# Kernel optimization log

Measured on AMD Instinct MI355X. Metric: run time of the kernel, lower is better.

## Reference

```python
import jax, jax.numpy as jnp
import numpy as np

DIM = 1024
HEADS = 16
HEAD_DIM = DIM // HEADS
SCALE = DIM ** -0.5  # note: original uses full dim, not head_dim


def setup_inputs() -> dict:
    key = jax.random.key(0)
    k1, k2, k3, k4 = jax.random.split(key, 4)
    x = jax.random.normal(k1, (4, 2048, DIM), dtype=jnp.float32)
    # nn.Linear(dim, 3*dim, bias=False): weight [3*dim, dim]; y = x @ W.T
    w_qkv = jax.random.normal(k2, (3 * DIM, DIM), dtype=jnp.float32) * (DIM ** -0.5)
    w_out = jax.random.normal(k3, (DIM, DIM), dtype=jnp.float32) * (DIM ** -0.5)
    b_out = jax.random.normal(k4, (DIM,), dtype=jnp.float32) * 0.01
    return {"x": x, "w_qkv": w_qkv, "w_out": w_out, "b_out": b_out}


def reference(x, w_qkv, w_out, b_out):
    b, n, d = x.shape
    qkv = jnp.einsum('bnd,ed->bne', x, w_qkv)  # [b, n, 3*dim]
    # rearrange 'b n (qkv h d) -> qkv b h n d'
    qkv = qkv.reshape(b, n, 3, HEADS, HEAD_DIM).transpose(2, 0, 3, 1, 4)
    q, k, v = qkv[0], qkv[1], qkv[2]
    dots = jnp.einsum('bhid,bhjd->bhij', q, k) * SCALE
    attn = jax.nn.softmax(dots, axis=-1)
    out = jnp.einsum('bhij,bhjd->bhid', attn, v)
    out = out.transpose(0, 2, 1, 3).reshape(b, n, d)  # b h n d -> b n (h d)
    return jnp.einsum('bnd,ed->bne', out, w_out) + b_out
```

## Files before the change

### kernel.cpp

```cpp
#include <hip/hip_runtime.h>
#include <stdint.h>
#include <stddef.h>

typedef _Float16 f16;
typedef __attribute__((ext_vector_type(8))) _Float16 f16x8;
typedef __attribute__((ext_vector_type(4))) _Float16 f16x4;
typedef __attribute__((ext_vector_type(2))) _Float16 f16x2;
typedef __attribute__((ext_vector_type(4))) float f32x4;

#define DINL __device__ __forceinline__

DINL f16x2 pkrtz(float a, float b) {
    return __builtin_bit_cast(f16x2, __builtin_amdgcn_cvt_pkrtz(a, b));
}

DINL void async_cp16(void* lds, const void* gmem) {
    __builtin_amdgcn_global_load_lds(
        (const __attribute__((address_space(1))) void*)(uintptr_t)gmem,
        (__attribute__((address_space(3))) void*)(uint32_t)(uintptr_t)lds,
        16, 0, 0);
}

__global__ void cast_fused(const float* __restrict__ x, f16* __restrict__ xh,
                           const float* __restrict__ wq, f16* __restrict__ wqh,
                           const float* __restrict__ wo, f16* __restrict__ woh,
                           float qs) {
    int stride = gridDim.x * blockDim.x;
    for (int i = blockIdx.x * blockDim.x + threadIdx.x; i < 3145728; i += stride) {
        const float4* src; f16x4* dst; float s = 1.f;
        if (i < 2097152)      { src = (const float4*)x  + i;            dst = (f16x4*)xh  + i; }
        else if (i < 2883584) { int j = i - 2097152; src = (const float4*)wq + j; dst = (f16x4*)wqh + j;
                                if (j < 262144) s = qs; }
        else                  { int j = i - 2883584; src = (const float4*)wo + j; dst = (f16x4*)woh + j; }
        float4 v = *src;
        f16x4 h = { (f16)(v.x * s), (f16)(v.y * s), (f16)(v.z * s), (f16)(v.w * s) };
        *dst = h;
    }
}

template <typename TC, bool HAS_BIAS>
__global__ __launch_bounds__(512, 2) void gemm8p(
    const f16* __restrict__ A, const f16* __restrict__ B,
    TC* __restrict__ C, const float* __restrict__ bias,
    int M, int N, int K)
{
    __shared__ __align__(16) char lds[98304];

    const int tid  = threadIdx.x;
    const int lane = tid & 63;
    const int wave = tid >> 6;
    const int rlo  = lane & 15;
    const int hi   = lane >> 4;
    const int wm   = wave & 3;
    const int wn   = wave >> 2;
    const int bm   = blockIdx.y * 256;
    const int bn   = blockIdx.x * 128;

    const int rA = tid >> 2;
    const int lc = (tid & 3) ^ ((tid >> 3) & 3);
    const f16* pA0 = A + (size_t)(bm + rA) * K + lc * 8;
    const f16* pA1 = A + (size_t)(bm + 128 + rA) * K + lc * 8;
    const f16* pB  = B + (size_t)(bn + rA) * K + lc * 8;
    const uint32_t dst0 = (uint32_t)tid * 16;
    const uint32_t dst1 = 8192u + (uint32_t)tid * 16;
    const uint32_t dstB = (uint32_t)tid * 16;

    const int fsw = (rlo >> 1) & 3;
    uint32_t afb[4], bfb[4];
#pragma unroll
    for (int m = 0; m < 4; ++m)
        afb[m] = (uint32_t)(wm * 64 + m * 16 + rlo) * 64 + (uint32_t)((hi ^ fsw) << 4);
#pragma unroll
    for (int n = 0; n < 4; ++n)
        bfb[n] = (uint32_t)(wn * 64 + n * 16 + rlo) * 64 + (uint32_t)((hi ^ fsw) << 4);

    f32x4 acc[4][4] = {};
    const int NP = K >> 5;

    auto stage = [&](int sg) {
        const uint32_t sa = (uint32_t)(sg & 3) << 14;
        const uint32_t sb = 65536u + ((uint32_t)(sg & 3) << 13);
        async_cp16(lds + sa + dst0, pA0);
        async_cp16(lds + sa + dst1, pA1);
        async_cp16(lds + sb + dstB, pB);
        pA0 += 32; pA1 += 32; pB += 32;
    };

    stage(0); stage(1); stage(2);

    for (int g = 0; g < NP; ++g) {
        if (g + 2 < NP)      asm volatile("s_waitcnt vmcnt(6)" ::: "memory");
        else if (g + 1 < NP) asm volatile("s_waitcnt vmcnt(3)" ::: "memory");
        else                 asm volatile("s_waitcnt vmcnt(0)" ::: "memory");
        __builtin_amdgcn_s_barrier();
        asm volatile("" ::: "memory");
        __builtin_amdgcn_sched_barrier(0);

        if (g + 3 < NP) stage(g + 3);

        const uint32_t sa = (uint32_t)(g & 3) << 14;
        const uint32_t sb = 65536u + ((uint32_t)(g & 3) << 13);

        f16x8 af[4], bf[4];
#pragma unroll
        for (int m = 0; m < 4; ++m)
            af[m] = *(const f16x8*)(lds + sa + afb[m]);
#pragma unroll
        for (int n = 0; n < 4; ++n)
            bf[n] = *(const f16x8*)(lds + sb + bfb[n]);

        __builtin_amdgcn_s_setprio(1);
#pragma unroll
        for (int m = 0; m < 4; ++m)
#pragma unroll
            for (int n = 0; n < 4; ++n)
                acc[m][n] = __builtin_amdgcn_mfma_f32_16x16x32_f16(af[m], bf[n], acc[m][n], 0, 0, 0);
        __builtin_amdgcn_s_setprio(0);
    }

#pragma unroll
    for (int n = 0; n < 4; ++n) {
        const int gc = bn + wn * 64 + n * 16 + rlo;
        float bv = 0.f;
        if constexpr (HAS_BIAS) bv = bias[gc];
#pragma unroll
        for (int m = 0; m < 4; ++m) {
            const int gr0 = bm + wm * 64 + m * 16 + (hi << 2);
#pragma unroll
            for (int r = 0; r < 4; ++r) {
                float v = acc[m][n][r] + bv;
                if constexpr (sizeof(TC) == 4) C[(size_t)(gr0 + r) * N + gc] = v;
                else                           C[(size_t)(gr0 + r) * N + gc] = (f16)v;
            }
        }
    }
}

__global__ __launch_bounds__(256) void transpose_v(const f16* __restrict__ qkv, f16* __restrict__ vt) {
    __shared__ float T[64][65];
    const int bid = blockIdx.x, bh = bid >> 5, st = bid & 31;
    const int b = bh >> 4, h = bh & 15, s0 = st * 64;
    const int tid = threadIdx.x;
    const int rs = tid >> 2, c0 = (tid & 3) * 16;
    const f16* src = &qkv[(size_t)(b * 2048 + s0 + rs) * 3072 + 2048 + h * 64 + c0];
    f16x8 v0 = ((const f16x8*)src)[0], v1 = ((const f16x8*)src)[1];
#pragma unroll
    for (int e = 0; e < 8; ++e) { T[rs][c0 + e] = (float)v0[e]; T[rs][c0 + 8 + e] = (float)v1[e]; }
    __syncthreads();
    const int rd = tid >> 2, k0 = (tid & 3) * 16;
    f16x8 w0, w1;
#pragma unroll
    for (int e = 0; e < 8; ++e) { w0[e] = (f16)T[k0 + e][rd]; w1[e] = (f16)T[k0 + 8 + e][rd]; }
    f16* dst = &vt[(size_t)(bh * 64 + rd) * 2048 + s0 + k0];
    ((f16x8*)dst)[0] = w0; ((f16x8*)dst)[1] = w1;
}

DINL int phi_row(int r) {
    return (r & 32) | ((r & 12) << 1) | ((r & 16) >> 2) | (r & 3);
}

__global__ __launch_bounds__(256, 4) void attn_mfma(
    const f16* __restrict__ qkv, const f16* __restrict__ vt, f16* __restrict__ out)
{
    constexpr int TD = 3072;
    constexpr int KSTR = 64 * TD;
    __shared__ __align__(16) f16 Ks[2][4096];
    __shared__ __align__(16) f16 Vs[3][4096];

    const int tid = threadIdx.x, lane = tid & 63, wave = tid >> 6;
    const int bh = blockIdx.x, b = bh >> 4, h = bh & 15;
    const int q0 = blockIdx.y * 128;
    const size_t base = (size_t)b * 2048 * TD + h * 64;
    const int lo = lane & 15, hi = lane >> 4;

    f16x8 qf[2][2];
#pragma unroll
    for (int g = 0; g < 2; ++g) {
        const f16* qp = &qkv[base + (size_t)(q0 + wave * 32 + g * 16 + lo) * TD + hi * 8];
        qf[g][0] = *(const f16x8*)qp;
        qf[g][1] = *(const f16x8*)(qp + 32);
    }

    const int s1 = tid,        r1 = s1 >> 3, c1 = (s1 & 7) ^ (r1 & 7);
    const int s2 = tid + 256,  r2 = s2 >> 3, c2 = (s2 & 7) ^ (r2 & 7);
    const f16* kg1 = &qkv[base + 1024 + (size_t)phi_row(r1) * TD + c1 * 8];
    const f16* kg2 = &qkv[base + 1024 + (size_t)phi_row(r2) * TD + c2 * 8];
    const f16* vg1 = &vt[(size_t)(bh * 64 + r1) * 2048 + c1 * 8];
    const f16* vg2 = &vt[(size_t)(bh * 64 + r2) * 2048 + c2 * 8];

    async_cp16(&Ks[0][s1 * 8], kg1); async_cp16(&Ks[0][s2 * 8], kg2);
    async_cp16(&Vs[0][s1 * 8], vg1); async_cp16(&Vs[0][s2 * 8], vg2);
    kg1 += KSTR; kg2 += KSTR; vg1 += 64; vg2 += 64;

    float lsum[2] = {};
    f32x4 o_[2][4] = {};
    union PaU { f16x8 v8[2]; f16x2 h2[8]; };
    PaU pa[2];

    for (int jt = 0; jt < 32; ++jt) {
        const int kc = jt & 1;
        __syncthreads();
        if (jt + 1 < 32) {
            const int kn = (jt + 1) & 1;
            const int vn = (jt + 1) % 3;
            async_cp16(&Ks[kn][s1 * 8], kg1); async_cp16(&Ks[kn][s2 * 8], kg2);
            async_cp16(&Vs[vn][s1 * 8], vg1); async_cp16(&Vs[vn][s2 * 8], vg2);
            kg1 += KSTR; kg2 += KSTR; vg1 += 64; vg2 += 64;
        }

        f32x4 sc[2][4] = {{}, {}};
        __builtin_amdgcn_s_setprio(1);
#pragma unroll
        for (int ks = 0; ks < 2; ++ks) {
            const int c = ks * 4 + hi;
#pragma unroll
            for (int n = 0; n < 4; ++n) {
                int kr = n * 16 + lo;
                f16x8 kf = *(const f16x8*)&Ks[kc][(kr * 8 + (c ^ (kr & 7))) * 8];
                sc[0][n] = __builtin_amdgcn_mfma_f32_16x16x32_f16(kf, qf[0][ks], sc[0][n], 0, 0, 0);
                sc[1][n] = __builtin_amdgcn_mfma_f32_16x16x32_f16(kf, qf[1][ks], sc[1][n], 0, 0, 0);
            }
        }
        __builtin_amdgcn_s_setprio(0);

        if (jt) {
            const int vp = (jt + 2) % 3;
            __builtin_amdgcn_s_setprio(1);
#pragma unroll
            for (int ks = 0; ks < 2; ++ks) {
                const int c = ks * 4 + hi;
#pragma unroll
                for (int n = 0; n < 4; ++n) {
                    int dd = n * 16 + lo;
                    f16x8 vb = *(const f16x8*)&Vs[vp][(dd * 8 + (c ^ (dd & 7))) * 8];
                    o_[0][n] = __builtin_amdgcn_mfma_f32_16x16x32_f16(pa[0].v8[ks], vb, o_[0][n], 0, 0, 0);
                    o_[1][n] = __builtin_amdgcn_mfma_f32_16x16x32_f16(pa[1].v8[ks], vb, o_[1][n], 0, 0, 0);
                }
            }
            __builtin_amdgcn_s_setprio(0);
        }

#pragma unroll
        for (int g = 0; g < 2; ++g)
#pragma unroll
        for (int n = 0; n < 4; ++n) {
            float p0 = exp2f(sc[g][n][0]), p1 = exp2f(sc[g][n][1]);
            float p2 = exp2f(sc[g][n][2]), p3 = exp2f(sc[g][n][3]);
            lsum[g] += (p0 + p1) + (p2 + p3);
            const int slot = (n >> 1) * 4 + (n & 1) * 2;
            pa[g].h2[slot]     = pkrtz(p0, p1);
            pa[g].h2[slot + 1] = pkrtz(p2, p3);
        }
    }

    {
        const int vp = 31 % 3;
#pragma unroll
        for (int ks = 0; ks < 2; ++ks) {
            const int c = ks * 4 + hi;
#pragma unroll
            for (int n = 0; n < 4; ++n) {
                int dd = n * 16 + lo;
                f16x8 vb = *(const f16x8*)&Vs[vp][(dd * 8 + (c ^ (dd & 7))) * 8];
                o_[0][n] = __builtin_amdgcn_mfma_f32_16x16x32_f16(pa[0].v8[ks], vb, o_[0][n], 0, 0, 0);
                o_[1][n] = __builtin_amdgcn_mfma_f32_16x16x32_f16(pa[1].v8[ks], vb, o_[1][n], 0, 0, 0);
            }
        }
    }

#pragma unroll
    for (int g = 0; g < 2; ++g) {
        float ls = lsum[g];
        ls += __shfl_xor(ls, 16);
        ls += __shfl_xor(ls, 32);
#pragma unroll
        for (int r = 0; r < 4; ++r) {
            float inv = 1.f / __shfl(ls, hi * 4 + r);
            int row = q0 + wave * 32 + g * 16 + hi * 4 + r;
#pragma unroll
            for (int n = 0; n < 4; ++n) {
                int dim = h * 64 + n * 16 + lo;
                out[(size_t)(b * 2048 + row) * 1024 + dim] = (f16)(o_[g][n][r] * inv);
            }
        }
    }
}

extern "C" void kernel_launch(void* const* d_in, const int* in_sizes, int n_in,
                              void* d_out, int out_size, void* d_ws, size_t ws_size,
                              hipStream_t stream)
{
    int ix = 0, iq = 1, iw = 2, ib = 3;
    for (int i = 0; i < n_in; ++i) {
        if      (in_sizes[i] == 8388608) ix = i;
        else if (in_sizes[i] == 3145728) iq = i;
        else if (in_sizes[i] == 1048576) iw = i;
        else if (in_sizes[i] == 1024)    ib = i;
    }
    const float* x     = (const float*)d_in[ix];
    const float* w_qkv = (const float*)d_in[iq];
    const float* w_out = (const float*)d_in[iw];
    const float* b_out = (const float*)d_in[ib];

    char* ws = (char*)d_ws;
    f16* Xh    = (f16*)(ws + 0);
    f16* AOh   = Xh;
    f16* Wqkvh = (f16*)(ws + 16777216);
    f16* QKVh  = (f16*)(ws + 23068672);
    f16* Vth   = (f16*)(ws + 73400320);
    f16* Wouth = (f16*)(ws + 90177536);

    const float QSCALE = 0.03125f * 1.4426950408889634f;

    cast_fused<<<3072, 256, 0, stream>>>(x, Xh, w_qkv, Wqkvh, w_out, Wouth, QSCALE);

    gemm8p<f16, false><<<dim3(24, 32), 512, 0, stream>>>(
        Xh, Wqkvh, QKVh, nullptr, 8192, 3072, 1024);

    transpose_v<<<2048, 256, 0, stream>>>(QKVh, Vth);

    attn_mfma<<<dim3(64, 16), 256, 0, stream>>>(QKVh, Vth, AOh);

    gemm8p<float, true><<<dim3(8, 32), 512, 0, stream>>>(
        AOh, Wouth, (float*)d_out, b_out, 8192, 1024, 1024);
}
```

Measured before the change: 309.3 us.

## Fuse V transpose into QKV GEMM epilogue and compute softmax sums via MFMA

The QKV GEMM epilogue now writes the V columns straight into the transposed V buffer as packed 4-element f16 stores, which removes the separate transpose_v kernel and its extra read and write of V. In attention, the per-row softmax denominator is accumulated with an extra MFMA against a vector of ones instead of scalar adds plus cross-lane shuffles. This adds two MFMAs per k-step and uses the fp16-rounded probabilities for the row sum. The V stores from the GEMM epilogue are strided 8-byte writes, which may coalesce poorly.

```diff
diff --git a/kernel.cpp b/kernel.cpp
--- a/kernel.cpp
+++ b/kernel.cpp
@@ -38,11 +38,11 @@
     }
 }
 
-template <typename TC, bool HAS_BIAS>
+template <typename TC, bool HAS_BIAS, bool FUSE_VT>
 __global__ __launch_bounds__(512, 2) void gemm8p(
     const f16* __restrict__ A, const f16* __restrict__ B,
     TC* __restrict__ C, const float* __restrict__ bias,
-    int M, int N, int K)
+    f16* __restrict__ VT, int M, int N, int K)
 {
     __shared__ __align__(16) char lds[98304];
 
@@ -118,41 +118,38 @@
         __builtin_amdgcn_s_setprio(0);
     }
 
-#pragma unroll
-    for (int n = 0; n < 4; ++n) {
-        const int gc = bn + wn * 64 + n * 16 + rlo;
-        float bv = 0.f;
-        if constexpr (HAS_BIAS) bv = bias[gc];
-#pragma unroll
-        for (int m = 0; m < 4; ++m) {
-            const int gr0 = bm + wm * 64 + m * 16 + (hi << 2);
-#pragma unroll
-            for (int r = 0; r < 4; ++r) {
-                float v = acc[m][n][r] + bv;
-                if constexpr (sizeof(TC) == 4) C[(size_t)(gr0 + r) * N + gc] = v;
-                else                           C[(size_t)(gr0 + r) * N + gc] = (f16)v;
-            }
-        }
-    }
-}
-
-__global__ __launch_bounds__(256) void transpose_v(const f16* __restrict__ qkv, f16* __restrict__ vt) {
-    __shared__ float T[64][65];
-    const int bid = blockIdx.x, bh = bid >> 5, st = bid & 31;
-    const int b = bh >> 4, h = bh & 15, s0 = st * 64;
-    const int tid = threadIdx.x;
-    const int rs = tid >> 2, c0 = (tid & 3) * 16;
-    const f16* src = &qkv[(size_t)(b * 2048 + s0 + rs) * 3072 + 2048 + h * 64 + c0];
-    f16x8 v0 = ((const f16x8*)src)[0], v1 = ((const f16x8*)src)[1];
-#pragma unroll
-    for (int e = 0; e < 8; ++e) { T[rs][c0 + e] = (float)v0[e]; T[rs][c0 + 8 + e] = (float)v1[e]; }
-    __syncthreads();
-    const int rd = tid >> 2, k0 = (tid & 3) * 16;
-    f16x8 w0, w1;
-#pragma unroll
-    for (int e = 0; e < 8; ++e) { w0[e] = (f16)T[k0 + e][rd]; w1[e] = (f16)T[k0 + 8 + e][rd]; }
-    f16* dst = &vt[(size_t)(bh * 64 + rd) * 2048 + s0 + k0];
-    ((f16x8*)dst)[0] = w0; ((f16x8*)dst)[1] = w1;
+    if (FUSE_VT && bn >= 2048) {
+#pragma unroll
+        for (int n = 0; n < 4; ++n) {
+            const int dh = bn + wn * 64 + n * 16 + rlo - 2048;
+            const int hh = dh >> 6, dd = dh & 63;
+#pragma unroll
+            for (int m = 0; m < 4; ++m) {
+                const int gr0 = bm + wm * 64 + m * 16 + (hi << 2);
+                const int bb = gr0 >> 11, seq = gr0 & 2047;
+                f16x4 v4 = { (f16)acc[m][n][0], (f16)acc[m][n][1],
+                             (f16)acc[m][n][2], (f16)acc[m][n][3] };
+                *(f16x4*)&VT[((size_t)((bb << 4) + hh) * 64 + dd) * 2048 + seq] = v4;
+            }
+        }
+    } else {
+#pragma unroll
+        for (int n = 0; n < 4; ++n) {
+            const int gc = bn + wn * 64 + n * 16 + rlo;
+            float bv = 0.f;
+            if constexpr (HAS_BIAS) bv = bias[gc];
+#pragma unroll
+            for (int m = 0; m < 4; ++m) {
+                const int gr0 = bm + wm * 64 + m * 16 + (hi << 2);
+#pragma unroll
+                for (int r = 0; r < 4; ++r) {
+                    float v = acc[m][n][r] + bv;
+                    if constexpr (sizeof(TC) == 4) C[(size_t)(gr0 + r) * N + gc] = v;
+                    else                           C[(size_t)(gr0 + r) * N + gc] = (f16)v;
+                }
+            }
+        }
+    }
 }
 
 DINL int phi_row(int r) {
@@ -192,8 +189,9 @@
     async_cp16(&Vs[0][s1 * 8], vg1); async_cp16(&Vs[0][s2 * 8], vg2);
     kg1 += KSTR; kg2 += KSTR; vg1 += 64; vg2 += 64;
 
-    float lsum[2] = {};
     f32x4 o_[2][4] = {};
+    f32x4 osum[2] = {};
+    const f16x8 vone = { (f16)1, (f16)1, (f16)1, (f16)1, (f16)1, (f16)1, (f16)1, (f16)1 };
     union PaU { f16x8 v8[2]; f16x2 h2[8]; };
     PaU pa[2];
 
@@ -236,6 +234,8 @@
                     o_[0][n] = __builtin_amdgcn_mfma_f32_16x16x32_f16(pa[0].v8[ks], vb, o_[0][n], 0, 0, 0);
                     o_[1][n] = __builtin_amdgcn_mfma_f32_16x16x32_f16(pa[1].v8[ks], vb, o_[1][n], 0, 0, 0);
                 }
+                osum[0] = __builtin_amdgcn_mfma_f32_16x16x32_f16(pa[0].v8[ks], vone, osum[0], 0, 0, 0);
+                osum[1] = __builtin_amdgcn_mfma_f32_16x16x32_f16(pa[1].v8[ks], vone, osum[1], 0, 0, 0);
             }
             __builtin_amdgcn_s_setprio(0);
         }
@@ -246,7 +246,6 @@
         for (int n = 0; n < 4; ++n) {
             float p0 = exp2f(sc[g][n][0]), p1 = exp2f(sc[g][n][1]);
             float p2 = exp2f(sc[g][n][2]), p3 = exp2f(sc[g][n][3]);
-            lsum[g] += (p0 + p1) + (p2 + p3);
             const int slot = (n >> 1) * 4 + (n & 1) * 2;
             pa[g].h2[slot]     = pkrtz(p0, p1);
             pa[g].h2[slot + 1] = pkrtz(p2, p3);
@@ -265,23 +264,21 @@
                 o_[0][n] = __builtin_amdgcn_mfma_f32_16x16x32_f16(pa[0].v8[ks], vb, o_[0][n], 0, 0, 0);
                 o_[1][n] = __builtin_amdgcn_mfma_f32_16x16x32_f16(pa[1].v8[ks], vb, o_[1][n], 0, 0, 0);
             }
-        }
-    }
-
-#pragma unroll
-    for (int g = 0; g < 2; ++g) {
-        float ls = lsum[g];
-        ls += __shfl_xor(ls, 16);
-        ls += __shfl_xor(ls, 32);
-#pragma unroll
-        for (int r = 0; r < 4; ++r) {
-            float inv = 1.f / __shfl(ls, hi * 4 + r);
-            int row = q0 + wave * 32 + g * 16 + hi * 4 + r;
-#pragma unroll
-            for (int n = 0; n < 4; ++n) {
-                int dim = h * 64 + n * 16 + lo;
-                out[(size_t)(b * 2048 + row) * 1024 + dim] = (f16)(o_[g][n][r] * inv);
-            }
+            osum[0] = __builtin_amdgcn_mfma_f32_16x16x32_f16(pa[0].v8[ks], vone, osum[0], 0, 0, 0);
+            osum[1] = __builtin_amdgcn_mfma_f32_16x16x32_f16(pa[1].v8[ks], vone, osum[1], 0, 0, 0);
+        }
+    }
+
+#pragma unroll
+    for (int g = 0; g < 2; ++g)
+#pragma unroll
+    for (int r = 0; r < 4; ++r) {
+        float inv = 1.f / osum[g][r];
+        int row = q0 + wave * 32 + g * 16 + hi * 4 + r;
+#pragma unroll
+        for (int n = 0; n < 4; ++n) {
+            int dim = h * 64 + n * 16 + lo;
+            out[(size_t)(b * 2048 + row) * 1024 + dim] = (f16)(o_[g][n][r] * inv);
         }
     }
 }
@@ -314,13 +311,11 @@
 
     cast_fused<<<3072, 256, 0, stream>>>(x, Xh, w_qkv, Wqkvh, w_out, Wouth, QSCALE);
 
-    gemm8p<f16, false><<<dim3(24, 32), 512, 0, stream>>>(
-        Xh, Wqkvh, QKVh, nullptr, 8192, 3072, 1024);
-
-    transpose_v<<<2048, 256, 0, stream>>>(QKVh, Vth);
+    gemm8p<f16, false, true><<<dim3(24, 32), 512, 0, stream>>>(
+        Xh, Wqkvh, QKVh, nullptr, Vth, 8192, 3072, 1024);
 
     attn_mfma<<<dim3(64, 16), 256, 0, stream>>>(QKVh, Vth, AOh);
 
-    gemm8p<float, true><<<dim3(8, 32), 512, 0, stream>>>(
-        AOh, Wouth, (float*)d_out, b_out, 8192, 1024, 1024);
-}
+    gemm8p<float, true, false><<<dim3(8, 32), 512, 0, stream>>>(
+        AOh, Wouth, (float*)d_out, b_out, nullptr, 8192, 1024, 1024);
+}
```

Result: slower. 321.4 us (+3.9%).
